# Performance work log

Measured on AMD Instinct MI355X. Metric: run time of the kernel, lower is better.

Reference implementation:

```python
import jax, jax.numpy as jnp
import numpy as np

MARGIN = 1.0


def _pairwise_sq_dist(emb):
    # squared euclidean distances, clamped at 0, diagonal zeroed (as in torch ref)
    ab = emb @ emb.T
    sq = jnp.diag(ab)
    d = jnp.maximum(sq[:, None] - 2.0 * ab + sq[None, :], 0.0)
    d = d * (d > 0.0).astype(d.dtype)  # error_mask step (faithful)
    B = d.shape[0]
    return d * (1.0 - jnp.eye(B, dtype=d.dtype))


def setup_inputs() -> dict:
    key = jax.random.key(0)
    k1, k2 = jax.random.split(key)
    emb = jax.random.normal(k1, (512, 256), dtype=jnp.float32)
    labels = jax.random.randint(k2, (512,), 0, 64, dtype=jnp.int64)
    return {"input": emb, "target": labels}


def reference(input, target):
    emb = input.astype(jnp.float32)
    pd = _pairwise_sq_dist(emb)                      # [B, B]
    B = pd.shape[0]
    adj = target[:, None] == target[None, :]         # [B, B]
    adj_not = ~adj

    # mask3[j, i, k]: negative k valid for anchor j w/ positive i (semi-hard: d(j,k) > d(j,i))
    mask3 = adj_not[:, None, :] & (pd[:, None, :] > pd[:, :, None])  # [B, B, B]

    # masked min over k: min of valid negatives, rowmax where masked out (torch trick equivalent)
    rowmax = pd.max(axis=1)                          # [B]
    negatives_outside = jnp.min(
        jnp.where(mask3, pd[:, None, :], rowmax[:, None, None]), axis=2
    )                                                # [B(anchor j), B(pos i)]

    # fallback: largest negative distance per anchor (masked max, rowmin where masked out)
    rowmin = pd.min(axis=1)                          # [B]
    negatives_inside = jnp.max(
        jnp.where(adj_not, pd, rowmin[:, None]), axis=1
    )                                                # [B]

    mask_final = jnp.any(mask3, axis=2)              # [B, B]
    semi_hard = jnp.where(mask_final, negatives_outside, negatives_inside[:, None])

    loss_mat = MARGIN + pd - semi_hard
    mask_pos = adj.astype(jnp.float32) - jnp.eye(B, dtype=jnp.float32)
    num_pos = mask_pos.sum()
    loss = jnp.maximum(loss_mat * mask_pos, 0.0).sum() / num_pos
    return loss.astype(input.dtype)
```

## Files before the change

kernel.cpp:

```cpp
#include <hip/hip_runtime.h>


#define BN 512
#define DF4 64

__device__ inline float wave_max64(float v){
  #pragma unroll
  for (int o = 32; o > 0; o >>= 1) v = fmaxf(v, __shfl_xor(v, o));
  return v;
}
__device__ inline float wave_min64(float v){
  #pragma unroll
  for (int o = 32; o > 0; o >>= 1) v = fminf(v, __shfl_xor(v, o));
  return v;
}

__global__ __launch_bounds__(256) void pd_gemm(
    const float* __restrict__ emb, float* __restrict__ pd, float* __restrict__ acc)
{
  __shared__ float As[32][260];
  __shared__ float Bs[32][260];
  __shared__ float sqA[32], sqB[32];
  __shared__ float outt[32][36];

  const int t  = threadIdx.x;
  const int bi = blockIdx.x & 15, bj = blockIdx.x >> 4;
  const int R0 = bi * 32, C0 = bj * 32;
  const float4* ef4 = reinterpret_cast<const float4*>(emb);

  if (blockIdx.x == 0 && t == 0){ acc[0] = 0.f; acc[1] = 0.f; ((int*)acc)[2] = 0; }

  #pragma unroll
  for (int j = 0; j < 8; ++j){
    int idx = t + j * 256;
    int r = idx >> 6, c = idx & 63;
    float4 va = ef4[(R0 + r) * DF4 + c];
    float4 vb = ef4[(C0 + r) * DF4 + c];
    *(float4*)&As[r][c * 4] = va;
    *(float4*)&Bs[r][c * 4] = vb;
  }
  {
    int half = t >> 7, u = t & 127;
    int r = u >> 2, part = u & 3;
    int base = ((half ? C0 : R0) + r) * DF4 + part * 16;
    float s = 0.f;
    #pragma unroll
    for (int i = 0; i < 16; ++i){
      float4 v = ef4[base + i];
      s += v.x*v.x + v.y*v.y + v.z*v.z + v.w*v.w;
    }
    s += __shfl_xor(s, 1); s += __shfl_xor(s, 2);
    if (part == 0){ if (half) sqB[r] = s; else sqA[r] = s; }
  }
  __syncthreads();

  const int r0 = t & 15, r1 = r0 + 16;
  const int c0 = t >> 4, c1 = c0 + 16;
  float a00 = 0.f, a01 = 0.f, a10 = 0.f, a11 = 0.f;
  #pragma unroll 8
  for (int kg = 0; kg < 64; ++kg){
    float4 A0 = *(const float4*)&As[r0][kg * 4];
    float4 A1 = *(const float4*)&As[r1][kg * 4];
    float4 B0 = *(const float4*)&Bs[c0][kg * 4];
    float4 B1 = *(const float4*)&Bs[c1][kg * 4];
    a00 += A0.x*B0.x + A0.y*B0.y + A0.z*B0.z + A0.w*B0.w;
    a01 += A0.x*B1.x + A0.y*B1.y + A0.z*B1.z + A0.w*B1.w;
    a10 += A1.x*B0.x + A1.y*B0.y + A1.z*B0.z + A1.w*B0.w;
    a11 += A1.x*B1.x + A1.y*B1.y + A1.z*B1.z + A1.w*B1.w;
  }

  const float sr0 = sqA[r0], sr1 = sqA[r1];
  const float sc0 = sqB[c0], sc1 = sqB[c1];
  float p00 = fmaxf(sr0 + sc0 - 2.f * a00, 0.f);
  float p01 = fmaxf(sr0 + sc1 - 2.f * a01, 0.f);
  float p10 = fmaxf(sr1 + sc0 - 2.f * a10, 0.f);
  float p11 = fmaxf(sr1 + sc1 - 2.f * a11, 0.f);
  if (bi == bj){
    if (r0 == c0) p00 = 0.f;
    if (r0 == c1) p01 = 0.f;
    if (r1 == c0) p10 = 0.f;
    if (r1 == c1) p11 = 0.f;
  }
  outt[r0][c0] = p00; outt[r0][c1] = p01;
  outt[r1][c0] = p10; outt[r1][c1] = p11;
  __syncthreads();

  int rr = t >> 3, cc = t & 7;
  float4 v = *(float4*)&outt[rr][cc * 4];
  *(float4*)&pd[(R0 + rr) * BN + C0 + cc * 4] = v;
}

__global__ __launch_bounds__(256) void mining(
    const float* __restrict__ pd, const int* __restrict__ labels,
    float* __restrict__ acc, float* __restrict__ out)
{
  __shared__ float wls[4], wcs[4];
  const int t = threadIdx.x, lane = t & 63, wid = t >> 6;
  const int j  = blockIdx.x * 4 + wid;
  const int lj = labels[j];

  const float4* prow = reinterpret_cast<const float4*>(pd + (size_t)j * BN);
  const int4*   lrow = reinterpret_cast<const int4*>(labels);
  float4 p0 = prow[lane * 2], p1 = prow[lane * 2 + 1];
  int4   l0 = lrow[lane * 2], l1 = lrow[lane * 2 + 1];
  float pk[8] = {p0.x, p0.y, p0.z, p0.w, p1.x, p1.y, p1.z, p1.w};
  int   lk[8] = {l0.x, l0.y, l0.z, l0.w, l1.x, l1.y, l1.z, l1.w};
  const int kbase = lane * 8;

  float ninside = 0.f;
  #pragma unroll
  for (int m = 0; m < 8; ++m)
    if (lk[m] != lj) ninside = fmaxf(ninside, pk[m]);
  ninside = wave_max64(ninside);

  float lsum = 0.f; int pcnt = 0;
  #pragma unroll
  for (int m = 0; m < 8; ++m){
    unsigned long long bal = __ballot(lk[m] == lj && (kbase + m) != j);
    while (bal){
      int L = (int)__ffsll((unsigned long long)bal) - 1;
      bal &= bal - 1;
      float tiv = __shfl(pk[m], L);
      float vmin = 3.402823466e38f;
      #pragma unroll
      for (int mm = 0; mm < 8; ++mm)
        if (lk[mm] != lj && pk[mm] > tiv) vmin = fminf(vmin, pk[mm]);
      vmin = wave_min64(vmin);
      float semi = (vmin < 3.0e38f) ? vmin : ninside;
      lsum += fmaxf(1.0f + tiv - semi, 0.f);
      ++pcnt;
    }
  }

  if (lane == 0){ wls[wid] = lsum; wcs[wid] = (float)pcnt; }
  __syncthreads();
  if (t == 0){
    float bl = wls[0] + wls[1] + wls[2] + wls[3];
    float bc = wcs[0] + wcs[1] + wcs[2] + wcs[3];
    atomicAdd(&acc[0], bl);
    atomicAdd(&acc[1], bc);
    __threadfence();
    int tk = atomicAdd((int*)acc + 2, 1);
    if (tk == 127){
      __threadfence();
      float tot = atomicAdd(&acc[0], 0.f);
      float cnt = atomicAdd(&acc[1], 0.f);
      out[0] = tot / cnt;
    }
  }
}

extern "C" void kernel_launch(void* const* d_in, const int* in_sizes, int n_in,
                              void* d_out, int out_size, void* d_ws, size_t ws_size,
                              hipStream_t stream) {
  const float* emb    = (const float*)d_in[0];
  const int*   labels = (const int*)d_in[1];
  float* out = (float*)d_out;
  float* pdw = (float*)d_ws;
  float* acc = pdw + BN * BN;
  pd_gemm<<<256, 256, 0, stream>>>(emb, pdw, acc);
  mining<<<128, 256, 0, stream>>>(pdw, labels, acc, out);
}
```

Measured before the change: 72.71 us.

## Fuse distance GEMM and mining into one cooperative kernel with grid sync

Merges the pairwise-distance GEMM and the semi-hard mining pass into a single cooperative kernel separated by a grid-wide barrier, with each of 256 blocks mining two anchor rows using two of its four waves. This removes the second kernel launch and the gap between launches. In exchange it adds a grid sync, leaves half the waves idle during mining, and falls back to the two-kernel path if the cooperative launch fails.

```diff
diff --git a/kernel.cpp b/kernel.cpp
--- a/kernel.cpp
+++ b/kernel.cpp
@@ -1,4 +1,7 @@
 #include <hip/hip_runtime.h>
+#include <hip/hip_cooperative_groups.h>
+
+namespace cg = cooperative_groups;
 
 
 #define BN 512
@@ -13,6 +16,142 @@
   #pragma unroll
   for (int o = 32; o > 0; o >>= 1) v = fminf(v, __shfl_xor(v, o));
   return v;
+}
+
+__global__ __launch_bounds__(256) void triplet_fused(
+    const float* __restrict__ emb, const int* __restrict__ labels,
+    float* __restrict__ pd, float* __restrict__ acc, float* __restrict__ out)
+{
+  __shared__ float As[32][260];
+  __shared__ float Bs[32][260];
+  __shared__ float sqA[32], sqB[32];
+  __shared__ float outt[32][36];
+  __shared__ float wls[2], wcs[2];
+
+  const int t  = threadIdx.x;
+  const int bi = blockIdx.x & 15, bj = blockIdx.x >> 4;
+  const int R0 = bi * 32, C0 = bj * 32;
+  const float4* ef4 = reinterpret_cast<const float4*>(emb);
+
+  if (blockIdx.x == 0 && t == 0){ acc[0] = 0.f; acc[1] = 0.f; ((int*)acc)[2] = 0; }
+
+  #pragma unroll
+  for (int j = 0; j < 8; ++j){
+    int idx = t + j * 256;
+    int r = idx >> 6, c = idx & 63;
+    float4 va = ef4[(R0 + r) * DF4 + c];
+    float4 vb = ef4[(C0 + r) * DF4 + c];
+    *(float4*)&As[r][c * 4] = va;
+    *(float4*)&Bs[r][c * 4] = vb;
+  }
+  {
+    int half = t >> 7, u = t & 127;
+    int r = u >> 2, part = u & 3;
+    int base = ((half ? C0 : R0) + r) * DF4 + part * 16;
+    float s = 0.f;
+    #pragma unroll
+    for (int i = 0; i < 16; ++i){
+      float4 v = ef4[base + i];
+      s += v.x*v.x + v.y*v.y + v.z*v.z + v.w*v.w;
+    }
+    s += __shfl_xor(s, 1); s += __shfl_xor(s, 2);
+    if (part == 0){ if (half) sqB[r] = s; else sqA[r] = s; }
+  }
+  __syncthreads();
+
+  const int r0 = t & 15, r1 = r0 + 16;
+  const int c0 = t >> 4, c1 = c0 + 16;
+  float a00 = 0.f, a01 = 0.f, a10 = 0.f, a11 = 0.f;
+  #pragma unroll 8
+  for (int kg = 0; kg < 64; ++kg){
+    float4 A0 = *(const float4*)&As[r0][kg * 4];
+    float4 A1 = *(const float4*)&As[r1][kg * 4];
+    float4 B0 = *(const float4*)&Bs[c0][kg * 4];
+    float4 B1 = *(const float4*)&Bs[c1][kg * 4];
+    a00 += A0.x*B0.x + A0.y*B0.y + A0.z*B0.z + A0.w*B0.w;
+    a01 += A0.x*B1.x + A0.y*B1.y + A0.z*B1.z + A0.w*B1.w;
+    a10 += A1.x*B0.x + A1.y*B0.y + A1.z*B0.z + A1.w*B0.w;
+    a11 += A1.x*B1.x + A1.y*B1.y + A1.z*B1.z + A1.w*B1.w;
+  }
+
+  const float sr0 = sqA[r0], sr1 = sqA[r1];
+  const float sc0 = sqB[c0], sc1 = sqB[c1];
+  float p00 = fmaxf(sr0 + sc0 - 2.f * a00, 0.f);
+  float p01 = fmaxf(sr0 + sc1 - 2.f * a01, 0.f);
+  float p10 = fmaxf(sr1 + sc0 - 2.f * a10, 0.f);
+  float p11 = fmaxf(sr1 + sc1 - 2.f * a11, 0.f);
+  if (bi == bj){
+    if (r0 == c0) p00 = 0.f;
+    if (r0 == c1) p01 = 0.f;
+    if (r1 == c0) p10 = 0.f;
+    if (r1 == c1) p11 = 0.f;
+  }
+  outt[r0][c0] = p00; outt[r0][c1] = p01;
+  outt[r1][c0] = p10; outt[r1][c1] = p11;
+  __syncthreads();
+
+  int rr = t >> 3, cc = t & 7;
+  float4 v = *(float4*)&outt[rr][cc * 4];
+  *(float4*)&pd[(R0 + rr) * BN + C0 + cc * 4] = v;
+
+  __threadfence();
+  cg::this_grid().sync();
+  __threadfence();
+
+  const int lane = t & 63, wid = t >> 6;
+  if (wid < 2){
+    const int j  = blockIdx.x * 2 + wid;
+    const int lj = labels[j];
+
+    const float4* prow = reinterpret_cast<const float4*>(pd + (size_t)j * BN);
+    const int4*   lrow = reinterpret_cast<const int4*>(labels);
+    float4 p0 = prow[lane * 2], p1 = prow[lane * 2 + 1];
+    int4   l0 = lrow[lane * 2], l1 = lrow[lane * 2 + 1];
+    float pk[8] = {p0.x, p0.y, p0.z, p0.w, p1.x, p1.y, p1.z, p1.w};
+    int   lk[8] = {l0.x, l0.y, l0.z, l0.w, l1.x, l1.y, l1.z, l1.w};
+    const int kbase = lane * 8;
+
+    float ninside = 0.f;
+    #pragma unroll
+    for (int m = 0; m < 8; ++m)
+      if (lk[m] != lj) ninside = fmaxf(ninside, pk[m]);
+    ninside = wave_max64(ninside);
+
+    float lsum = 0.f; int pcnt = 0;
+    #pragma unroll
+    for (int m = 0; m < 8; ++m){
+      unsigned long long bal = __ballot(lk[m] == lj && (kbase + m) != j);
+      while (bal){
+        int L = (int)__ffsll((unsigned long long)bal) - 1;
+        bal &= bal - 1;
+        float tiv = __shfl(pk[m], L);
+        float vmin = 3.402823466e38f;
+        #pragma unroll
+        for (int mm = 0; mm < 8; ++mm)
+          if (lk[mm] != lj && pk[mm] > tiv) vmin = fminf(vmin, pk[mm]);
+        vmin = wave_min64(vmin);
+        float semi = (vmin < 3.0e38f) ? vmin : ninside;
+        lsum += fmaxf(1.0f + tiv - semi, 0.f);
+        ++pcnt;
+      }
+    }
+    if (lane == 0){ wls[wid] = lsum; wcs[wid] = (float)pcnt; }
+  }
+  __syncthreads();
+  if (t == 0){
+    float bl = wls[0] + wls[1];
+    float bc = wcs[0] + wcs[1];
+    atomicAdd(&acc[0], bl);
+    atomicAdd(&acc[1], bc);
+    __threadfence();
+    int tk = atomicAdd((int*)acc + 2, 1);
+    if (tk == 255){
+      __threadfence();
+      float tot = atomicAdd(&acc[0], 0.f);
+      float cnt = atomicAdd(&acc[1], 0.f);
+      out[0] = tot / cnt;
+    }
+  }
 }
 
 __global__ __launch_bounds__(256) void pd_gemm(
@@ -158,6 +297,12 @@
   float* out = (float*)d_out;
   float* pdw = (float*)d_ws;
   float* acc = pdw + BN * BN;
-  pd_gemm<<<256, 256, 0, stream>>>(emb, pdw, acc);
-  mining<<<128, 256, 0, stream>>>(pdw, labels, acc, out);
-}
+
+  void* args[5] = { (void*)&emb, (void*)&labels, (void*)&pdw, (void*)&acc, (void*)&out };
+  hipError_t e = hipLaunchCooperativeKernel((const void*)triplet_fused,
+                                            dim3(256), dim3(256), args, 0, stream);
+  if (e != hipSuccess){
+    pd_gemm<<<256, 256, 0, stream>>>(emb, pdw, acc);
+    mining<<<128, 256, 0, stream>>>(pdw, labels, acc, out);
+  }
+}
```

After: 137.0 us. 88.4% more time.

## Fuse distance GEMM and mining into one kernel with grid barrier

Applied to the files above, without the earlier changes.

Merges the pairwise-distance kernel and the semi-hard mining kernel into a single launch. A global atomic counter with a generation scheme acts as a grid-wide barrier between the two phases. Each of the 256 blocks then mines 2 anchor rows using 2 of its 4 waves. This removes the second kernel launch and its inter-kernel gap. In exchange it relies on all 256 blocks being co-resident for the spin barrier to be deadlock-free, and leaves half the waves idle during mining.

```diff
diff --git a/kernel.cpp b/kernel.cpp
--- a/kernel.cpp
+++ b/kernel.cpp
@@ -3,6 +3,8 @@
 
 #define BN 512
 #define DF4 64
+
+__device__ unsigned int g_bar = 0;
 
 __device__ inline float wave_max64(float v){
   #pragma unroll
@@ -15,13 +17,15 @@
   return v;
 }
 
-__global__ __launch_bounds__(256) void pd_gemm(
-    const float* __restrict__ emb, float* __restrict__ pd, float* __restrict__ acc)
+__global__ __launch_bounds__(256) void triplet_fused(
+    const float* __restrict__ emb, const int* __restrict__ labels,
+    float* __restrict__ pd, float* __restrict__ acc, float* __restrict__ out)
 {
   __shared__ float As[32][260];
   __shared__ float Bs[32][260];
   __shared__ float sqA[32], sqB[32];
   __shared__ float outt[32][36];
+  __shared__ float wls[2], wcs[2];
 
   const int t  = threadIdx.x;
   const int bi = blockIdx.x & 15, bj = blockIdx.x >> 4;
@@ -88,60 +92,66 @@
   int rr = t >> 3, cc = t & 7;
   float4 v = *(float4*)&outt[rr][cc * 4];
   *(float4*)&pd[(R0 + rr) * BN + C0 + cc * 4] = v;
-}
 
-__global__ __launch_bounds__(256) void mining(
-    const float* __restrict__ pd, const int* __restrict__ labels,
-    float* __restrict__ acc, float* __restrict__ out)
-{
-  __shared__ float wls[4], wcs[4];
-  const int t = threadIdx.x, lane = t & 63, wid = t >> 6;
-  const int j  = blockIdx.x * 4 + wid;
-  const int lj = labels[j];
-
-  const float4* prow = reinterpret_cast<const float4*>(pd + (size_t)j * BN);
-  const int4*   lrow = reinterpret_cast<const int4*>(labels);
-  float4 p0 = prow[lane * 2], p1 = prow[lane * 2 + 1];
-  int4   l0 = lrow[lane * 2], l1 = lrow[lane * 2 + 1];
-  float pk[8] = {p0.x, p0.y, p0.z, p0.w, p1.x, p1.y, p1.z, p1.w};
-  int   lk[8] = {l0.x, l0.y, l0.z, l0.w, l1.x, l1.y, l1.z, l1.w};
-  const int kbase = lane * 8;
-
-  float ninside = 0.f;
-  #pragma unroll
-  for (int m = 0; m < 8; ++m)
-    if (lk[m] != lj) ninside = fmaxf(ninside, pk[m]);
-  ninside = wave_max64(ninside);
-
-  float lsum = 0.f; int pcnt = 0;
-  #pragma unroll
-  for (int m = 0; m < 8; ++m){
-    unsigned long long bal = __ballot(lk[m] == lj && (kbase + m) != j);
-    while (bal){
-      int L = (int)__ffsll((unsigned long long)bal) - 1;
-      bal &= bal - 1;
-      float tiv = __shfl(pk[m], L);
-      float vmin = 3.402823466e38f;
-      #pragma unroll
-      for (int mm = 0; mm < 8; ++mm)
-        if (lk[mm] != lj && pk[mm] > tiv) vmin = fminf(vmin, pk[mm]);
-      vmin = wave_min64(vmin);
-      float semi = (vmin < 3.0e38f) ? vmin : ninside;
-      lsum += fmaxf(1.0f + tiv - semi, 0.f);
-      ++pcnt;
-    }
-  }
-
-  if (lane == 0){ wls[wid] = lsum; wcs[wid] = (float)pcnt; }
   __syncthreads();
   if (t == 0){
-    float bl = wls[0] + wls[1] + wls[2] + wls[3];
-    float bc = wcs[0] + wcs[1] + wcs[2] + wcs[3];
+    __threadfence();
+    unsigned old = atomicAdd(&g_bar, 1u);
+    unsigned target = ((old >> 8) + 1u) << 8;
+    while (__hip_atomic_load(&g_bar, __ATOMIC_RELAXED, __HIP_MEMORY_SCOPE_AGENT) < target)
+      __builtin_amdgcn_s_sleep(1);
+  }
+  __syncthreads();
+  __threadfence();
+
+  const int lane = t & 63, wid = t >> 6;
+  if (wid < 2){
+    const int j  = blockIdx.x * 2 + wid;
+    const int lj = labels[j];
+
+    const float4* prow = reinterpret_cast<const float4*>(pd + (size_t)j * BN);
+    const int4*   lrow = reinterpret_cast<const int4*>(labels);
+    float4 p0 = prow[lane * 2], p1 = prow[lane * 2 + 1];
+    int4   l0 = lrow[lane * 2], l1 = lrow[lane * 2 + 1];
+    float pk[8] = {p0.x, p0.y, p0.z, p0.w, p1.x, p1.y, p1.z, p1.w};
+    int   lk[8] = {l0.x, l0.y, l0.z, l0.w, l1.x, l1.y, l1.z, l1.w};
+    const int kbase = lane * 8;
+
+    float ninside = 0.f;
+    #pragma unroll
+    for (int m = 0; m < 8; ++m)
+      if (lk[m] != lj) ninside = fmaxf(ninside, pk[m]);
+    ninside = wave_max64(ninside);
+
+    float lsum = 0.f; int pcnt = 0;
+    #pragma unroll
+    for (int m = 0; m < 8; ++m){
+      unsigned long long bal = __ballot(lk[m] == lj && (kbase + m) != j);
+      while (bal){
+        int L = (int)__ffsll((unsigned long long)bal) - 1;
+        bal &= bal - 1;
+        float tiv = __shfl(pk[m], L);
+        float vmin = 3.402823466e38f;
+        #pragma unroll
+        for (int mm = 0; mm < 8; ++mm)
+          if (lk[mm] != lj && pk[mm] > tiv) vmin = fminf(vmin, pk[mm]);
+        vmin = wave_min64(vmin);
+        float semi = (vmin < 3.0e38f) ? vmin : ninside;
+        lsum += fmaxf(1.0f + tiv - semi, 0.f);
+        ++pcnt;
+      }
+    }
+    if (lane == 0){ wls[wid] = lsum; wcs[wid] = (float)pcnt; }
+  }
+  __syncthreads();
+  if (t == 0){
+    float bl = wls[0] + wls[1];
+    float bc = wcs[0] + wcs[1];
     atomicAdd(&acc[0], bl);
     atomicAdd(&acc[1], bc);
     __threadfence();
     int tk = atomicAdd((int*)acc + 2, 1);
-    if (tk == 127){
+    if (tk == 255){
       __threadfence();
       float tot = atomicAdd(&acc[0], 0.f);
       float cnt = atomicAdd(&acc[1], 0.f);
@@ -158,6 +168,6 @@
   float* out = (float*)d_out;
   float* pdw = (float*)d_ws;
   float* acc = pdw + BN * BN;
-  pd_gemm<<<256, 256, 0, stream>>>(emb, pdw, acc);
-  mining<<<128, 256, 0, stream>>>(pdw, labels, acc, out);
+
+  triplet_fused<<<256, 256, 0, stream>>>(emb, labels, pdw, acc, out);
 }
```

New measurement: 104.1 us. +43.2%, slower.
